# Kernel optimization log

Measured on AMD Instinct MI355X. Metric: run time of the kernel, lower is better.

The kernel has to match this reference:

```python
import jax, jax.numpy as jnp
import numpy as np

H, DH = 16, 64  # n_head, head_dim


def setup_inputs() -> dict:
    key = jax.random.key(0)
    ks = jax.random.split(key, 14)
    B, L, D = 2, 1024, 1024
    d = DH

    def lin_w(k, fan_in, shape):
        return jax.random.normal(k, shape, jnp.float32) / np.sqrt(fan_in)

    return {
        "x": jax.random.normal(ks[0], (B, L, D), jnp.float32),
        "Wq": lin_w(ks[1], D, (D, D)),
        "bq": jnp.zeros((D,), jnp.float32),
        "Wk1": lin_w(ks[2], D, (D, D)),
        "bk1": jnp.zeros((D,), jnp.float32),
        "Wk2": lin_w(ks[3], D, (D, D)),
        "bk2": jnp.zeros((D,), jnp.float32),
        "Wg": lin_w(ks[4], d, (d, 1)),
        "bg": jnp.zeros((1,), jnp.float32),
        "Ws": lin_w(ks[5], d, (d, 1)),
        "bs": jnp.zeros((1,), jnp.float32),
        "Wp": lin_w(ks[6], D, (D, D)),
        "bp": jnp.zeros((D,), jnp.float32),
    }


def reference(x, Wq, bq, Wk1, bk1, Wk2, bk2, Wg, bg, Ws, bs, Wp, bp):
    B, L, D = x.shape
    d = DH
    # AR (GLA) branch
    Q = (x @ Wq + bq).reshape(B, L, H, d)
    K = (x @ Wk1 + bk1).reshape(B, L, H, d)
    V = x.reshape(B, L, H, d)
    W = jnp.einsum('blhd,blhe->blhde', K, V)  # (B,L,H,d,d) outer products
    # stable cumprod of sigmoid gate via log-cumsum-exp trick
    G = jax.nn.sigmoid(x.reshape(B, L, H, d) @ Wg + bg)            # (B,L,H,1)
    log_cum = jnp.clip(jnp.cumsum(jnp.log(jnp.clip(G, 1e-6, None)), axis=1), -30.0, 30.0)
    Gc = (jnp.exp(log_cum) + 1e-6)[..., None]                       # (B,L,H,1,1)
    R = jax.nn.silu(K @ Ws + bs)[..., None]                         # (B,L,H,1,1) decay gate
    Wc = jnp.cumsum(W * R / Gc, axis=1) * Gc                        # weighted cumsum
    O1 = jnp.einsum('blhd,blhde->blhe', Q, Wc)                      # (B,L,H,d)
    # MA branch on one-step residuals
    E = V[:, 1:] - O1[:, :-1]                                       # (B,L-1,H,d)
    q2 = -jax.nn.leaky_relu(-Q[:, :-1] / np.sqrt(d), 0.02)          # ma_q_activation (scale head_dim)
    k2 = jax.nn.sigmoid((x[:, :-1] @ Wk2 + bk2) / np.sqrt(D) * 0.02)  # ma_k_activation (scale n_embd)
    k2 = k2.reshape(B, L - 1, H, d)
    W_ma = jnp.cumsum(jnp.einsum('blhd,blhe->blhde', k2, E), axis=1)
    O2 = jnp.einsum('blhd,blhde->blhe', q2, W_ma)
    O2 = jnp.concatenate([jnp.zeros_like(O2[:, :1]), O2], axis=1)   # shift: first MA output is 0
    O = (O1 + O2).reshape(B, L, D)
    return O @ Wp + bp
```

## Files before the change

### kernel.cpp

```cpp
#include <hip/hip_runtime.h>
#include <hip/hip_bf16.h>
#include <math.h>

#define B_  2
#define L_  1024
#define D_  1024
#define H_  16
#define DH_ 64
#define M_  (B_*L_)
#define CHUNK 64
#define NCH (L_/CHUNK)
#define PT 72
#define PS 76

#define KSCALE (0.02f/32.0f)

using bf16x8 = __attribute__((ext_vector_type(8))) short;
using f32x4  = __attribute__((ext_vector_type(4))) float;

__device__ __forceinline__ unsigned short bf16r(float f){
  union{float f; unsigned int u;} x; x.f = f;
  unsigned int r = x.u + 0x7FFF + ((x.u>>16)&1);
  return (unsigned short)(r>>16);
}
__device__ __forceinline__ float bf2f(unsigned short u){
  union{unsigned int u; float f;} x; x.u = ((unsigned int)u)<<16; return x.f;
}

__global__ __launch_bounds__(256) void convert_all(
  const float* __restrict__ X,
  const float* __restrict__ W0, const float* __restrict__ W1,
  const float* __restrict__ W2, const float* __restrict__ W3,
  unsigned short* __restrict__ Xbf,
  unsigned short* __restrict__ T0, unsigned short* __restrict__ T1,
  unsigned short* __restrict__ T2, unsigned short* __restrict__ T3)
{
  int z = blockIdx.z;
  if (z == 4) {
    int row = blockIdx.x*64 + (threadIdx.x>>2);
    int col = blockIdx.y*64 + (threadIdx.x&3)*16;
    const float4* src = (const float4*)&X[(size_t)row*D_ + col];
    float4 a=src[0], b=src[1], c=src[2], d=src[3];
    unsigned short buf[16] = {
      bf16r(a.x),bf16r(a.y),bf16r(a.z),bf16r(a.w),
      bf16r(b.x),bf16r(b.y),bf16r(b.z),bf16r(b.w),
      bf16r(c.x),bf16r(c.y),bf16r(c.z),bf16r(c.w),
      bf16r(d.x),bf16r(d.y),bf16r(d.z),bf16r(d.w)};
    *(uint4*)&Xbf[(size_t)row*D_ + col]     = *(uint4*)&buf[0];
    *(uint4*)&Xbf[(size_t)row*D_ + col + 8] = *(uint4*)&buf[8];
    return;
  }
  if (blockIdx.x >= 16) return;
  const float* W = z==0?W0: z==1?W1: z==2?W2: W3;
  unsigned short* T = z==0?T0: z==1?T1: z==2?T2: T3;
  __shared__ float tile[64][65];
  int kBase = blockIdx.x*64, nBase = blockIdx.y*64;
  #pragma unroll
  for (int i=0;i<16;i++){
    int idx = threadIdx.x + i*256;
    int r = idx>>6, c = idx&63;
    tile[r][c] = W[(size_t)(kBase+r)*D_ + nBase+c];
  }
  __syncthreads();
  #pragma unroll
  for (int i=0;i<16;i++){
    int idx = threadIdx.x + i*256;
    int n = idx>>6, k = idx&63;
    T[(size_t)(nBase+n)*D_ + kBase+k] = bf16r(tile[k][n]);
  }
}

__global__ __launch_bounds__(256) void gemm3(
  const unsigned short* __restrict__ A,
  const unsigned short* __restrict__ T0, const unsigned short* __restrict__ T1,
  const unsigned short* __restrict__ T2,
  const float* __restrict__ b0, const float* __restrict__ b1, const float* __restrict__ b2,
  unsigned short* __restrict__ F0, unsigned short* __restrict__ F1,
  unsigned short* __restrict__ F2)
{
  int z = blockIdx.z;
  const unsigned short* Bt = z==0?T0: z==1?T1: T2;
  const float* bias = z==0?b0: z==1?b1: b2;
  unsigned short* F = z==0?F0: z==1?F1: F2;
  int epi = (z==2) ? 1 : 0;
  int rowBase = blockIdx.x*128, colBase = blockIdx.y*128;

  __shared__ __align__(16) unsigned short As[128*32];
  __shared__ __align__(16) unsigned short Bs[128*32];
  int tid = threadIdx.x, w = tid>>6, l = tid&63;
  int lr = l&15, g4 = l>>4;
  int wr = w>>1, wc = w&1;
  f32x4 acc[4][4];
  #pragma unroll
  for (int mi=0;mi<4;mi++)
    #pragma unroll
    for (int ni=0;ni<4;ni++)
      acc[mi][ni] = (f32x4){0.f,0.f,0.f,0.f};

  for (int k0 = 0; k0 < D_; k0 += 32) {
    #pragma unroll
    for (int i=0;i<2;i++){
      int Fi = (w*2+i)*64 + l;
      int r = Fi>>2, c16 = Fi&3;
      int sc = c16 ^ ((r>>1)&3);
      const unsigned short* ga = A  + (size_t)(rowBase+r)*D_ + k0 + sc*8;
      const unsigned short* gb = Bt + (size_t)(colBase+r)*D_ + k0 + sc*8;
      __builtin_amdgcn_global_load_lds(
        (const __attribute__((address_space(1))) void*)ga,
        (__attribute__((address_space(3))) void*)(As + (size_t)(w*2+i)*512), 16, 0, 0);
      __builtin_amdgcn_global_load_lds(
        (const __attribute__((address_space(1))) void*)gb,
        (__attribute__((address_space(3))) void*)(Bs + (size_t)(w*2+i)*512), 16, 0, 0);
    }
    __syncthreads();
    bf16x8 af[4], bfr[4];
    #pragma unroll
    for (int mi=0;mi<4;mi++){
      int row = wr*64 + mi*16 + lr;
      af[mi] = *(const bf16x8*)(As + row*32 + ((g4 ^ ((row>>1)&3))*8));
    }
    #pragma unroll
    for (int ni=0;ni<4;ni++){
      int n = wc*64 + ni*16 + lr;
      bfr[ni] = *(const bf16x8*)(Bs + n*32 + ((g4 ^ ((n>>1)&3))*8));
    }
    #pragma unroll
    for (int mi=0;mi<4;mi++)
      #pragma unroll
      for (int ni=0;ni<4;ni++)
        acc[mi][ni] = __builtin_amdgcn_mfma_f32_16x16x32_bf16(af[mi], bfr[ni], acc[mi][ni], 0,0,0);
    __syncthreads();
  }

  #pragma unroll
  for (int mi=0;mi<4;mi++){
    #pragma unroll
    for (int ni=0;ni<4;ni++){
      int col = colBase + wc*64 + ni*16 + lr;
      float bv = bias[col];
      #pragma unroll
      for (int r=0;r<4;r++){
        int row = rowBase + wr*64 + mi*16 + g4*4 + r;
        float v = acc[mi][ni][r] + bv;
        if (epi) v = 1.f/(1.f + expf(-v*KSCALE));
        F[(size_t)row*D_ + col] = bf16r(v);
      }
    }
  }
}

__global__ __launch_bounds__(256) void gemm1(
  const unsigned short* __restrict__ A, const unsigned short* __restrict__ Bt,
  const float* __restrict__ bias, float* __restrict__ C)
{
  int rowBase = blockIdx.x*128, colBase = blockIdx.y*64;
  __shared__ __align__(16) unsigned short As[128*32];
  __shared__ __align__(16) unsigned short Bs[64*32];
  int tid = threadIdx.x, w = tid>>6, l = tid&63;
  int lr = l&15, g4 = l>>4;
  f32x4 acc[2][4];
  #pragma unroll
  for (int mi=0;mi<2;mi++)
    #pragma unroll
    for (int ni=0;ni<4;ni++)
      acc[mi][ni] = (f32x4){0.f,0.f,0.f,0.f};

  for (int k0 = 0; k0 < D_; k0 += 32) {
    #pragma unroll
    for (int i=0;i<2;i++){
      int F = (w*2+i)*64 + l;
      int r = F>>2, c16 = F&3;
      int sc = c16 ^ ((r>>1)&3);
      const unsigned short* g = A + (size_t)(rowBase+r)*D_ + k0 + sc*8;
      __builtin_amdgcn_global_load_lds(
        (const __attribute__((address_space(1))) void*)g,
        (__attribute__((address_space(3))) void*)(As + (size_t)(w*2+i)*512), 16, 0, 0);
    }
    {
      int F = w*64 + l;
      int r = F>>2, c16 = F&3;
      int sc = c16 ^ ((r>>1)&3);
      const unsigned short* g = Bt + (size_t)(colBase+r)*D_ + k0 + sc*8;
      __builtin_amdgcn_global_load_lds(
        (const __attribute__((address_space(1))) void*)g,
        (__attribute__((address_space(3))) void*)(Bs + (size_t)w*512), 16, 0, 0);
    }
    __syncthreads();
    bf16x8 af[2], bfr[4];
    #pragma unroll
    for (int mi=0;mi<2;mi++){
      int row = w*32 + mi*16 + lr;
      af[mi] = *(const bf16x8*)(As + row*32 + ((g4 ^ ((row>>1)&3))*8));
    }
    #pragma unroll
    for (int ni=0;ni<4;ni++){
      int n = ni*16 + lr;
      bfr[ni] = *(const bf16x8*)(Bs + n*32 + ((g4 ^ ((n>>1)&3))*8));
    }
    #pragma unroll
    for (int mi=0;mi<2;mi++)
      #pragma unroll
      for (int ni=0;ni<4;ni++)
        acc[mi][ni] = __builtin_amdgcn_mfma_f32_16x16x32_bf16(af[mi], bfr[ni], acc[mi][ni], 0,0,0);
    __syncthreads();
  }

  #pragma unroll
  for (int mi=0;mi<2;mi++){
    #pragma unroll
    for (int ni=0;ni<4;ni++){
      int col = colBase + ni*16 + lr;
      float bv = bias[col];
      #pragma unroll
      for (int r=0;r<4;r++){
        int row = rowBase + w*32 + mi*16 + g4*4 + r;
        C[(size_t)row*D_ + col] = acc[mi][ni][r] + bv;
      }
    }
  }
}

__global__ __launch_bounds__(256) void scalars_kernel(
  const float* __restrict__ X, const unsigned short* __restrict__ Kbf,
  const float* __restrict__ Wg, const float* __restrict__ bg,
  const float* __restrict__ Ws, const float* __restrict__ bs,
  float* __restrict__ GL, float* __restrict__ RR)
{
  int item = blockIdx.x * 4 + (threadIdx.x >> 6);
  int ln = threadIdx.x & 63;
  int row = item >> 4;
  int h = item & 15;
  float xv = X[(size_t)row*D_ + h*64 + ln];
  float kv = bf2f(Kbf[(size_t)row*D_ + h*64 + ln]);
  float gdot = xv * Wg[ln];
  float rdot = kv * Ws[ln];
  #pragma unroll
  for (int off = 32; off; off >>= 1) {
    gdot += __shfl_xor(gdot, off);
    rdot += __shfl_xor(rdot, off);
  }
  if (ln == 0) {
    float glogit = gdot + bg[0];
    float sg = 1.f/(1.f+expf(-glogit));
    sg = fmaxf(sg, 1e-6f);
    GL[item] = logf(sg);
    float rlogit = rdot + bs[0];
    RR[item] = rlogit / (1.f + expf(-rlogit));
  }
}

__global__ __launch_bounds__(256) void gl_scan(
  const float* __restrict__ GL, const float* __restrict__ RR,
  float* __restrict__ GC, float* __restrict__ CF)
{
  int bh = blockIdx.x * 4 + (threadIdx.x >> 6);
  int b = bh >> 4, h = bh & 15;
  int ln = threadIdx.x & 63;
  float carry = 0.f;
  for (int it = 0; it < 16; ++it) {
    int l = it*64 + ln;
    float x = GL[((size_t)(b*L_ + l))*H_ + h];
    #pragma unroll
    for (int off = 1; off < 64; off <<= 1) {
      float t = __shfl_up(x, off);
      if (ln >= off) x += t;
    }
    float tot = __shfl(x, 63);
    float cum = carry + x;
    carry += tot;
    float lc = fminf(fmaxf(cum, -30.f), 30.f);
    float gc = expf(lc) + 1e-6f;
    GC[(size_t)bh*L_ + l] = gc;
    CF[(size_t)bh*L_ + l] = RR[((size_t)(b*L_ + l))*H_ + h] / gc;
  }
}

__global__ __launch_bounds__(256) void ar_chunk_sum(
  const unsigned short* __restrict__ Kbf, const unsigned short* __restrict__ Xbf,
  const float* __restrict__ CF, float* __restrict__ CS)
{
  int bh = blockIdx.x, c = blockIdx.y;
  int b = bh >> 4, h = bh & 15;
  int row0 = b*L_ + c*CHUNK;
  __shared__ __align__(16) unsigned short kt_t[64*PT];
  __shared__ __align__(16) unsigned short cv_t[64*PT];
  __shared__ __align__(16) float uni[64*PS];
  __shared__ float cf_s[64];
  int tid = threadIdx.x;
  if (tid < 64) cf_s[tid] = CF[(size_t)bh*L_ + c*CHUNK + tid];
  __syncthreads();
  const unsigned short* kg = Kbf + (size_t)row0*D_ + h*64;
  const unsigned short* vg = Xbf + (size_t)row0*D_ + h*64;
  #pragma unroll
  for (int t=0;t<2;t++){
    int j = (tid>>3) + t*32;
    int d0 = (tid&7)*8;
    bf16x8 kv = *(const bf16x8*)&kg[(size_t)j*D_ + d0];
    bf16x8 vv = *(const bf16x8*)&vg[(size_t)j*D_ + d0];
    float cfj = cf_s[j];
    #pragma unroll
    for (int i=0;i<8;i++){
      kt_t[(d0+i)*PT + j] = (unsigned short)kv[i];
      cv_t[(d0+i)*PT + j] = bf16r(bf2f((unsigned short)vv[i]) * cfj);
    }
  }
  __syncthreads();
  int w = tid>>6, l = tid&63, lr = l&15, g4 = l>>4;
  f32x4 acc[4];
  #pragma unroll
  for (int ni=0;ni<4;ni++) acc[ni] = (f32x4){0.f,0.f,0.f,0.f};
  #pragma unroll
  for (int kk=0;kk<2;kk++){
    bf16x8 a = *(const bf16x8*)&cv_t[(w*16+lr)*PT + kk*32 + g4*8];
    #pragma unroll
    for (int ni=0;ni<4;ni++){
      bf16x8 bb = *(const bf16x8*)&kt_t[(ni*16+lr)*PT + kk*32 + g4*8];
      acc[ni] = __builtin_amdgcn_mfma_f32_16x16x32_bf16(a, bb, acc[ni], 0,0,0);
    }
  }
  #pragma unroll
  for (int ni=0;ni<4;ni++)
    #pragma unroll
    for (int r=0;r<4;r++)
      uni[(w*16+g4*4+r)*PS + ni*16+lr] = acc[ni][r];
  __syncthreads();
  float* out = CS + ((size_t)bh*NCH + c)*4096;
  #pragma unroll
  for (int t=0;t<4;t++){
    int idx = tid + t*256;
    int r = idx>>4, s = idx&15;
    *(float4*)&out[r*64 + s*4] = *(float4*)&uni[r*PS + s*4];
  }
}

__global__ __launch_bounds__(256) void ma_chunk_sum(
  const unsigned short* __restrict__ K2bf, const unsigned short* __restrict__ Xbf,
  const float* __restrict__ O1, float* __restrict__ CS)
{
  int bh = blockIdx.x, c = blockIdx.y;
  int b = bh >> 4, h = bh & 15;
  int row0 = b*L_ + c*CHUNK;
  __shared__ __align__(16) unsigned short kt_t[64*PT];
  __shared__ __align__(16) unsigned short et_t[64*PT];
  __shared__ __align__(16) float uni[64*PS];
  int tid = threadIdx.x;
  const unsigned short* kg = K2bf + (size_t)row0*D_ + h*64;
  #pragma unroll
  for (int t=0;t<2;t++){
    int j = (tid>>3) + t*32;
    int e0 = (tid&7)*8;
    bf16x8 kv = *(const bf16x8*)&kg[(size_t)j*D_ + e0];
    float ev[8] = {0.f,0.f,0.f,0.f,0.f,0.f,0.f,0.f};
    if (c*CHUNK + j < L_-1){
      bf16x8 xv = *(const bf16x8*)&Xbf[(size_t)(row0+j+1)*D_ + h*64 + e0];
      const float4* op = (const float4*)&O1[(size_t)(row0+j)*D_ + h*64 + e0];
      float4 o0 = op[0], o1v = op[1];
      ev[0]=bf2f((unsigned short)xv[0])-o0.x;  ev[1]=bf2f((unsigned short)xv[1])-o0.y;
      ev[2]=bf2f((unsigned short)xv[2])-o0.z;  ev[3]=bf2f((unsigned short)xv[3])-o0.w;
      ev[4]=bf2f((unsigned short)xv[4])-o1v.x; ev[5]=bf2f((unsigned short)xv[5])-o1v.y;
      ev[6]=bf2f((unsigned short)xv[6])-o1v.z; ev[7]=bf2f((unsigned short)xv[7])-o1v.w;
    }
    #pragma unroll
    for (int i=0;i<8;i++){
      kt_t[(e0+i)*PT + j] = (unsigned short)kv[i];
      et_t[(e0+i)*PT + j] = bf16r(ev[i]);
    }
  }
  __syncthreads();
  int w = tid>>6, l = tid&63, lr = l&15, g4 = l>>4;
  f32x4 acc[4];
  #pragma unroll
  for (int ni=0;ni<4;ni++) acc[ni] = (f32x4){0.f,0.f,0.f,0.f};
  #pragma unroll
  for (int kk=0;kk<2;kk++){
    bf16x8 a = *(const bf16x8*)&et_t[(w*16+lr)*PT + kk*32 + g4*8];
    #pragma unroll
    for (int ni=0;ni<4;ni++){
      bf16x8 bb = *(const bf16x8*)&kt_t[(ni*16+lr)*PT + kk*32 + g4*8];
      acc[ni] = __builtin_amdgcn_mfma_f32_16x16x32_bf16(a, bb, acc[ni], 0,0,0);
    }
  }
  #pragma unroll
  for (int ni=0;ni<4;ni++)
    #pragma unroll
    for (int r=0;r<4;r++)
      uni[(w*16+g4*4+r)*PS + ni*16+lr] = acc[ni][r];
  __syncthreads();
  float* out = CS + ((size_t)bh*NCH + c)*4096;
  #pragma unroll
  for (int t=0;t<4;t++){
    int idx = tid + t*256;
    int r = idx>>4, s = idx&15;
    *(float4*)&out[r*64 + s*4] = *(float4*)&uni[r*PS + s*4];
  }
}

__global__ __launch_bounds__(256) void ar_o1_mfma(
  const unsigned short* __restrict__ Qbf, const unsigned short* __restrict__ Kbf,
  const unsigned short* __restrict__ Xbf, const float* __restrict__ CF,
  const float* __restrict__ GC, const float* __restrict__ CS,
  float* __restrict__ O1)
{
  int bh = blockIdx.x, c = blockIdx.y;
  int b = bh >> 4, h = bh & 15;
  int row0 = b*L_ + c*CHUNK;
  __shared__ __align__(16) unsigned short q_t[64*PT];
  __shared__ __align__(16) unsigned short k_t[64*PT];
  __shared__ __align__(16) unsigned short vt_t[64*PT];
  __shared__ __align__(16) unsigned short st_t[64*PT];
  __shared__ __align__(16) float uni[64*PS];
  unsigned short* p_t = (unsigned short*)uni;
  __shared__ float cf_s[64], gc_s[64];
  int tid = threadIdx.x;
  if (tid < 64) {
    cf_s[tid] = CF[(size_t)bh*L_ + c*CHUNK + tid];
    gc_s[tid] = GC[(size_t)bh*L_ + c*CHUNK + tid];
  }
  const unsigned short* qg = Qbf + (size_t)row0*D_ + h*64;
  const unsigned short* kg = Kbf + (size_t)row0*D_ + h*64;
  const unsigned short* vg = Xbf + (size_t)row0*D_ + h*64;
  const float* csb = CS + (size_t)bh*NCH*4096;
  {
    float carry[16];
    #pragma unroll
    for (int i=0;i<16;i++) carry[i] = 0.f;
    const float* cb = csb + (size_t)tid*16;
    for (int c2=0;c2<c;c2++){
      const float4* p4 = (const float4*)(cb + (size_t)c2*4096);
      float4 a0=p4[0],a1=p4[1],a2=p4[2],a3=p4[3];
      carry[0]+=a0.x; carry[1]+=a0.y; carry[2]+=a0.z; carry[3]+=a0.w;
      carry[4]+=a1.x; carry[5]+=a1.y; carry[6]+=a1.z; carry[7]+=a1.w;
      carry[8]+=a2.x; carry[9]+=a2.y; carry[10]+=a2.z; carry[11]+=a2.w;
      carry[12]+=a3.x; carry[13]+=a3.y; carry[14]+=a3.z; carry[15]+=a3.w;
    }
    unsigned short buf[16];
    #pragma unroll
    for (int i=0;i<16;i++) buf[i] = bf16r(carry[i]);
    int row = tid>>2, col = (tid&3)*16;
    *(uint4*)&st_t[row*PT + col]     = *(uint4*)&buf[0];
    *(uint4*)&st_t[row*PT + col + 8] = *(uint4*)&buf[8];
  }
  #pragma unroll
  for (int t=0;t<2;t++){
    int idx = tid + t*256;
    int j = idx>>3, s = idx&7;
    *(uint4*)&q_t[j*PT + s*8] = *(const uint4*)&qg[(size_t)j*D_ + s*8];
    *(uint4*)&k_t[j*PT + s*8] = *(const uint4*)&kg[(size_t)j*D_ + s*8];
  }
  #pragma unroll
  for (int t=0;t<2;t++){
    int j = (tid>>3) + t*32;
    int e0 = (tid&7)*8;
    bf16x8 vv = *(const bf16x8*)&vg[(size_t)j*D_ + e0];
    #pragma unroll
    for (int i=0;i<8;i++) vt_t[(e0+i)*PT + j] = (unsigned short)vv[i];
  }
  __syncthreads();
  int w = tid>>6, l = tid&63, lr = l&15, g4 = l>>4;
  f32x4 acc[4];
  #pragma unroll
  for (int ni=0;ni<4;ni++) acc[ni] = (f32x4){0.f,0.f,0.f,0.f};
  #pragma unroll
  for (int kk=0;kk<2;kk++){
    bf16x8 a = *(const bf16x8*)&q_t[(w*16+lr)*PT + kk*32 + g4*8];
    #pragma unroll
    for (int ni=0;ni<4;ni++){
      bf16x8 bb = *(const bf16x8*)&k_t[(ni*16+lr)*PT + kk*32 + g4*8];
      acc[ni] = __builtin_amdgcn_mfma_f32_16x16x32_bf16(a, bb, acc[ni], 0,0,0);
    }
  }
  #pragma unroll
  for (int ni=0;ni<4;ni++){
    int j = ni*16 + lr;
    float cf = cf_s[j];
    #pragma unroll
    for (int r=0;r<4;r++){
      int row = w*16 + g4*4 + r;
      float v = (j <= row) ? acc[ni][r]*cf : 0.f;
      p_t[row*PT + j] = bf16r(v);
    }
  }
  __syncthreads();
  #pragma unroll
  for (int ni=0;ni<4;ni++) acc[ni] = (f32x4){0.f,0.f,0.f,0.f};
  #pragma unroll
  for (int kk=0;kk<2;kk++){
    bf16x8 ap = *(const bf16x8*)&p_t[(w*16+lr)*PT + kk*32 + g4*8];
    bf16x8 aq = *(const bf16x8*)&q_t[(w*16+lr)*PT + kk*32 + g4*8];
    #pragma unroll
    for (int ni=0;ni<4;ni++){
      bf16x8 bv = *(const bf16x8*)&vt_t[(ni*16+lr)*PT + kk*32 + g4*8];
      bf16x8 bs = *(const bf16x8*)&st_t[(ni*16+lr)*PT + kk*32 + g4*8];
      acc[ni] = __builtin_amdgcn_mfma_f32_16x16x32_bf16(ap, bv, acc[ni], 0,0,0);
      acc[ni] = __builtin_amdgcn_mfma_f32_16x16x32_bf16(aq, bs, acc[ni], 0,0,0);
    }
  }
  __syncthreads();
  #pragma unroll
  for (int ni=0;ni<4;ni++)
    #pragma unroll
    for (int r=0;r<4;r++){
      int row = w*16 + g4*4 + r;
      uni[row*PS + ni*16 + lr] = gc_s[row]*acc[ni][r];
    }
  __syncthreads();
  #pragma unroll
  for (int t=0;t<4;t++){
    int idx = tid + t*256;
    int r = idx>>4, s = idx&15;
    *(float4*)&O1[(size_t)(row0+r)*D_ + h*64 + s*4] = *(float4*)&uni[r*PS + s*4];
  }
}

__global__ __launch_bounds__(256) void ma_o2_mfma(
  const unsigned short* __restrict__ Qbf, const unsigned short* __restrict__ K2bf,
  const unsigned short* __restrict__ Xbf, const float* __restrict__ CS,
  const float* __restrict__ O1, unsigned short* __restrict__ Obf)
{
  int bh = blockIdx.x, c = blockIdx.y;
  int b = bh >> 4, h = bh & 15;
  int row0 = b*L_ + c*CHUNK;
  __shared__ __align__(16) unsigned short q_t[64*PT];
  __shared__ __align__(16) unsigned short k_t[64*PT];
  __shared__ __align__(16) unsigned short et_t[64*PT];
  __shared__ __align__(16) unsigned short tt_t[64*PT];
  __shared__ __align__(16) float uni[64*PS];
  unsigned short* p_t = (unsigned short*)uni;
  int tid = threadIdx.x;
  const unsigned short* qg = Qbf  + (size_t)row0*D_ + h*64;
  const unsigned short* kg = K2bf + (size_t)row0*D_ + h*64;
  const float* csb = CS + (size_t)bh*NCH*4096;
  {
    float carry[16];
    #pragma unroll
    for (int i=0;i<16;i++) carry[i] = 0.f;
    const float* cb = csb + (size_t)tid*16;
    for (int c2=0;c2<c;c2++){
      const float4* p4 = (const float4*)(cb + (size_t)c2*4096);
      float4 a0=p4[0],a1=p4[1],a2=p4[2],a3=p4[3];
      carry[0]+=a0.x; carry[1]+=a0.y; carry[2]+=a0.z; carry[3]+=a0.w;
      carry[4]+=a1.x; carry[5]+=a1.y; carry[6]+=a1.z; carry[7]+=a1.w;
      carry[8]+=a2.x; carry[9]+=a2.y; carry[10]+=a2.z; carry[11]+=a2.w;
      carry[12]+=a3.x; carry[13]+=a3.y; carry[14]+=a3.z; carry[15]+=a3.w;
    }
    unsigned short buf[16];
    #pragma unroll
    for (int i=0;i<16;i++) buf[i] = bf16r(carry[i]);
    int row = tid>>2, col = (tid&3)*16;
    *(uint4*)&tt_t[row*PT + col]     = *(uint4*)&buf[0];
    *(uint4*)&tt_t[row*PT + col + 8] = *(uint4*)&buf[8];
  }
  #pragma unroll
  for (int t=0;t<2;t++){
    int idx = tid + t*256;
    int j = idx>>3, s = idx&7;
    *(uint4*)&k_t[j*PT + s*8] = *(const uint4*)&kg[(size_t)j*D_ + s*8];
  }
  #pragma unroll
  for (int t=0;t<2;t++){
    int j = (tid>>3) + t*32;
    int d0 = (tid&7)*8;
    bf16x8 qv = *(const bf16x8*)&qg[(size_t)j*D_ + d0];
    unsigned short qb[8];
    #pragma unroll
    for (int i=0;i<8;i++){
      float q = bf2f((unsigned short)qv[i]);
      qb[i] = bf16r((q > 0.f ? 0.02f*q : q) * 0.125f);
    }
    *(uint4*)&q_t[j*PT + d0] = *(uint4*)&qb[0];
    float ev[8] = {0.f,0.f,0.f,0.f,0.f,0.f,0.f,0.f};
    if (c*CHUNK + j < L_-1){
      bf16x8 xv = *(const bf16x8*)&Xbf[(size_t)(row0+j+1)*D_ + h*64 + d0];
      const float4* op = (const float4*)&O1[(size_t)(row0+j)*D_ + h*64 + d0];
      float4 o0 = op[0], o1v = op[1];
      ev[0]=bf2f((unsigned short)xv[0])-o0.x;  ev[1]=bf2f((unsigned short)xv[1])-o0.y;
      ev[2]=bf2f((unsigned short)xv[2])-o0.z;  ev[3]=bf2f((unsigned short)xv[3])-o0.w;
      ev[4]=bf2f((unsigned short)xv[4])-o1v.x; ev[5]=bf2f((unsigned short)xv[5])-o1v.y;
      ev[6]=bf2f((unsigned short)xv[6])-o1v.z; ev[7]=bf2f((unsigned short)xv[7])-o1v.w;
    }
    #pragma unroll
    for (int i=0;i<8;i++) et_t[(d0+i)*PT + j] = bf16r(ev[i]);
  }
  __syncthreads();
  int w = tid>>6, l = tid&63, lr = l&15, g4 = l>>4;
  f32x4 acc[4];
  #pragma unroll
  for (int ni=0;ni<4;ni++) acc[ni] = (f32x4){0.f,0.f,0.f,0.f};
  #pragma unroll
  for (int kk=0;kk<2;kk++){
    bf16x8 a = *(const bf16x8*)&q_t[(w*16+lr)*PT + kk*32 + g4*8];
    #pragma unroll
    for (int ni=0;ni<4;ni++){
      bf16x8 bb = *(const bf16x8*)&k_t[(ni*16+lr)*PT + kk*32 + g4*8];
      acc[ni] = __builtin_amdgcn_mfma_f32_16x16x32_bf16(a, bb, acc[ni], 0,0,0);
    }
  }
  #pragma unroll
  for (int ni=0;ni<4;ni++){
    int j = ni*16 + lr;
    #pragma unroll
    for (int r=0;r<4;r++){
      int row = w*16 + g4*4 + r;
      float v = (j <= row) ? acc[ni][r] : 0.f;
      p_t[row*PT + j] = bf16r(v);
    }
  }
  __syncthreads();
  #pragma unroll
  for (int ni=0;ni<4;ni++) acc[ni] = (f32x4){0.f,0.f,0.f,0.f};
  #pragma unroll
  for (int kk=0;kk<2;kk++){
    bf16x8 ap = *(const bf16x8*)&p_t[(w*16+lr)*PT + kk*32 + g4*8];
    bf16x8 aq = *(const bf16x8*)&q_t[(w*16+lr)*PT + kk*32 + g4*8];
    #pragma unroll
    for (int ni=0;ni<4;ni++){
      bf16x8 be = *(const bf16x8*)&et_t[(ni*16+lr)*PT + kk*32 + g4*8];
      bf16x8 bt = *(const bf16x8*)&tt_t[(ni*16+lr)*PT + kk*32 + g4*8];
      acc[ni] = __builtin_amdgcn_mfma_f32_16x16x32_bf16(ap, be, acc[ni], 0,0,0);
      acc[ni] = __builtin_amdgcn_mfma_f32_16x16x32_bf16(aq, bt, acc[ni], 0,0,0);
    }
  }
  __syncthreads();
  #pragma unroll
  for (int ni=0;ni<4;ni++)
    #pragma unroll
    for (int r=0;r<4;r++){
      int row = w*16 + g4*4 + r;
      uni[row*PS + ni*16 + lr] = acc[ni][r];
    }
  __syncthreads();
  #pragma unroll
  for (int t=0;t<4;t++){
    int idx = tid + t*256;
    int r = idx>>4, s = idx&15;
    if (c*CHUNK + r < L_-1) {
      const float4 gv = *(const float4*)&O1[(size_t)(row0+r+1)*D_ + h*64 + s*4];
      float4 uv = *(float4*)&uni[r*PS + s*4];
      ushort4 o;
      o.x = bf16r(gv.x+uv.x); o.y = bf16r(gv.y+uv.y);
      o.z = bf16r(gv.z+uv.z); o.w = bf16r(gv.w+uv.w);
      *(ushort4*)&Obf[(size_t)(row0+r+1)*D_ + h*64 + s*4] = o;
    }
  }
  if (c == 0 && tid < 16) {
    const float4 gv = *(const float4*)&O1[(size_t)row0*D_ + h*64 + tid*4];
    ushort4 o;
    o.x = bf16r(gv.x); o.y = bf16r(gv.y); o.z = bf16r(gv.z); o.w = bf16r(gv.w);
    *(ushort4*)&Obf[(size_t)row0*D_ + h*64 + tid*4] = o;
  }
}

extern "C" void kernel_launch(void* const* d_in, const int* in_sizes, int n_in,
                              void* d_out, int out_size, void* d_ws, size_t ws_size,
                              hipStream_t stream) {
  const float* x  = (const float*)d_in[0];
  const float* Wq = (const float*)d_in[1];
  const float* bq = (const float*)d_in[2];
  const float* Wk1= (const float*)d_in[3];
  const float* bk1= (const float*)d_in[4];
  const float* Wk2= (const float*)d_in[5];
  const float* bk2= (const float*)d_in[6];
  const float* Wg = (const float*)d_in[7];
  const float* bg = (const float*)d_in[8];
  const float* Ws = (const float*)d_in[9];
  const float* bs = (const float*)d_in[10];
  const float* Wp = (const float*)d_in[11];
  const float* bp = (const float*)d_in[12];
  float* out = (float*)d_out;

  float* ws = (float*)d_ws;
  size_t MD = (size_t)M_*D_;
  float* O1b = ws;
  float* CSb = O1b + MD;
  float* GLb = CSb + (size_t)32*NCH*4096;
  float* RRb = GLb + (size_t)M_*H_;
  float* GCb = RRb + (size_t)M_*H_;
  float* CFb = GCb + (size_t)32*L_;
  unsigned short* Xbf   = (unsigned short*)(CFb + (size_t)32*L_);
  unsigned short* Qbfs  = Xbf  + MD;
  unsigned short* Kbfs  = Qbfs + MD;
  unsigned short* K2bfs = Kbfs + MD;
  unsigned short* Obf   = K2bfs+ MD;
  unsigned short* Wt0   = Obf + MD;
  unsigned short* Wt1   = Wt0 + (size_t)D_*D_;
  unsigned short* Wt2   = Wt1 + (size_t)D_*D_;
  unsigned short* Wt3   = Wt2 + (size_t)D_*D_;

  dim3 gcv(32, 16, 5);
  convert_all<<<gcv, 256, 0, stream>>>(x, Wq, Wk1, Wk2, Wp, Xbf, Wt0, Wt1, Wt2, Wt3);

  dim3 gg(M_/128, D_/128, 3);
  gemm3<<<gg, 256, 0, stream>>>(Xbf, Wt0, Wt1, Wt2, bq, bk1, bk2, Qbfs, Kbfs, K2bfs);

  scalars_kernel<<<(M_*H_)/4, 256, 0, stream>>>(x, Kbfs, Wg, bg, Ws, bs, GLb, RRb);
  gl_scan<<<8, 256, 0, stream>>>(GLb, RRb, GCb, CFb);

  dim3 gc(32, NCH);
  ar_chunk_sum<<<gc, 256, 0, stream>>>(Kbfs, Xbf, CFb, CSb);
  ar_o1_mfma<<<gc, 256, 0, stream>>>(Qbfs, Kbfs, Xbf, CFb, GCb, CSb, O1b);

  ma_chunk_sum<<<gc, 256, 0, stream>>>(K2bfs, Xbf, O1b, CSb);
  ma_o2_mfma<<<gc, 256, 0, stream>>>(Qbfs, K2bfs, Xbf, CSb, O1b, Obf);

  dim3 go(M_/128, D_/64);
  gemm1<<<go, 256, 0, stream>>>(Obf, Wt3, bp, out);
}
```

Measured before the change: 184.7 us.

## Fold gate scan into chunk kernels and fuse MA chunk sums into AR output

Removes the separate gate-scan kernel. Each chunk block now recomputes its own gate prefix, with one warp reducing the earlier chunks' log-gates, and GL/RR are stored head-major to make that read coalesced. The MA chunk-sum work moves into the AR output kernel, which builds the residual E from the O1 tile it already holds in shared memory instead of rereading O1 from global memory. This cuts two kernel launches and one global round trip of O1. In exchange, the prefix loop repeats work for later chunks and the fused kernel does more per block, with a longer serial tail.

```diff
diff --git a/kernel.cpp b/kernel.cpp
--- a/kernel.cpp
+++ b/kernel.cpp
@@ -25,6 +25,30 @@
 }
 __device__ __forceinline__ float bf2f(unsigned short u){
   union{unsigned int u; float f;} x; x.u = ((unsigned int)u)<<16; return x.f;
+}
+
+__device__ __forceinline__ void gate_prefix(
+  const float* __restrict__ GL, const float* __restrict__ RR,
+  int bh, int c, int l, float* cf_s, float* gc_s)
+{
+  float carry = 0.f;
+  for (int it = 0; it < c; ++it){
+    float g = GL[(size_t)bh*L_ + it*64 + l];
+    #pragma unroll
+    for (int off = 32; off; off >>= 1) g += __shfl_xor(g, off);
+    carry += g;
+  }
+  float x = GL[(size_t)bh*L_ + c*64 + l];
+  #pragma unroll
+  for (int off = 1; off < 64; off <<= 1){
+    float t = __shfl_up(x, off);
+    if (l >= off) x += t;
+  }
+  float cum = carry + x;
+  float lc = fminf(fmaxf(cum, -30.f), 30.f);
+  float gc = expf(lc) + 1e-6f;
+  cf_s[l] = RR[(size_t)bh*L_ + c*64 + l] / gc;
+  if (gc_s) gc_s[l] = gc;
 }
 
 __global__ __launch_bounds__(256) void convert_all(
@@ -240,44 +264,21 @@
     rdot += __shfl_xor(rdot, off);
   }
   if (ln == 0) {
+    int b = row >> 10, l = row & 1023;
+    size_t o = (size_t)(b*16 + h)*L_ + l;
     float glogit = gdot + bg[0];
     float sg = 1.f/(1.f+expf(-glogit));
     sg = fmaxf(sg, 1e-6f);
-    GL[item] = logf(sg);
+    GL[o] = logf(sg);
     float rlogit = rdot + bs[0];
-    RR[item] = rlogit / (1.f + expf(-rlogit));
-  }
-}
-
-__global__ __launch_bounds__(256) void gl_scan(
-  const float* __restrict__ GL, const float* __restrict__ RR,
-  float* __restrict__ GC, float* __restrict__ CF)
-{
-  int bh = blockIdx.x * 4 + (threadIdx.x >> 6);
-  int b = bh >> 4, h = bh & 15;
-  int ln = threadIdx.x & 63;
-  float carry = 0.f;
-  for (int it = 0; it < 16; ++it) {
-    int l = it*64 + ln;
-    float x = GL[((size_t)(b*L_ + l))*H_ + h];
-    #pragma unroll
-    for (int off = 1; off < 64; off <<= 1) {
-      float t = __shfl_up(x, off);
-      if (ln >= off) x += t;
-    }
-    float tot = __shfl(x, 63);
-    float cum = carry + x;
-    carry += tot;
-    float lc = fminf(fmaxf(cum, -30.f), 30.f);
-    float gc = expf(lc) + 1e-6f;
-    GC[(size_t)bh*L_ + l] = gc;
-    CF[(size_t)bh*L_ + l] = RR[((size_t)(b*L_ + l))*H_ + h] / gc;
+    RR[o] = rlogit / (1.f + expf(-rlogit));
   }
 }
 
 __global__ __launch_bounds__(256) void ar_chunk_sum(
   const unsigned short* __restrict__ Kbf, const unsigned short* __restrict__ Xbf,
-  const float* __restrict__ CF, float* __restrict__ CS)
+  const float* __restrict__ GL, const float* __restrict__ RR,
+  float* __restrict__ CS)
 {
   int bh = blockIdx.x, c = blockIdx.y;
   int b = bh >> 4, h = bh & 15;
@@ -287,7 +288,7 @@
   __shared__ __align__(16) float uni[64*PS];
   __shared__ float cf_s[64];
   int tid = threadIdx.x;
-  if (tid < 64) cf_s[tid] = CF[(size_t)bh*L_ + c*CHUNK + tid];
+  if (tid < 64) gate_prefix(GL, RR, bh, c, tid, cf_s, nullptr);
   __syncthreads();
   const unsigned short* kg = Kbf + (size_t)row0*D_ + h*64;
   const unsigned short* vg = Xbf + (size_t)row0*D_ + h*64;
@@ -333,72 +334,11 @@
   }
 }
 
-__global__ __launch_bounds__(256) void ma_chunk_sum(
-  const unsigned short* __restrict__ K2bf, const unsigned short* __restrict__ Xbf,
-  const float* __restrict__ O1, float* __restrict__ CS)
-{
-  int bh = blockIdx.x, c = blockIdx.y;
-  int b = bh >> 4, h = bh & 15;
-  int row0 = b*L_ + c*CHUNK;
-  __shared__ __align__(16) unsigned short kt_t[64*PT];
-  __shared__ __align__(16) unsigned short et_t[64*PT];
-  __shared__ __align__(16) float uni[64*PS];
-  int tid = threadIdx.x;
-  const unsigned short* kg = K2bf + (size_t)row0*D_ + h*64;
-  #pragma unroll
-  for (int t=0;t<2;t++){
-    int j = (tid>>3) + t*32;
-    int e0 = (tid&7)*8;
-    bf16x8 kv = *(const bf16x8*)&kg[(size_t)j*D_ + e0];
-    float ev[8] = {0.f,0.f,0.f,0.f,0.f,0.f,0.f,0.f};
-    if (c*CHUNK + j < L_-1){
-      bf16x8 xv = *(const bf16x8*)&Xbf[(size_t)(row0+j+1)*D_ + h*64 + e0];
-      const float4* op = (const float4*)&O1[(size_t)(row0+j)*D_ + h*64 + e0];
-      float4 o0 = op[0], o1v = op[1];
-      ev[0]=bf2f((unsigned short)xv[0])-o0.x;  ev[1]=bf2f((unsigned short)xv[1])-o0.y;
-      ev[2]=bf2f((unsigned short)xv[2])-o0.z;  ev[3]=bf2f((unsigned short)xv[3])-o0.w;
-      ev[4]=bf2f((unsigned short)xv[4])-o1v.x; ev[5]=bf2f((unsigned short)xv[5])-o1v.y;
-      ev[6]=bf2f((unsigned short)xv[6])-o1v.z; ev[7]=bf2f((unsigned short)xv[7])-o1v.w;
-    }
-    #pragma unroll
-    for (int i=0;i<8;i++){
-      kt_t[(e0+i)*PT + j] = (unsigned short)kv[i];
-      et_t[(e0+i)*PT + j] = bf16r(ev[i]);
-    }
-  }
-  __syncthreads();
-  int w = tid>>6, l = tid&63, lr = l&15, g4 = l>>4;
-  f32x4 acc[4];
-  #pragma unroll
-  for (int ni=0;ni<4;ni++) acc[ni] = (f32x4){0.f,0.f,0.f,0.f};
-  #pragma unroll
-  for (int kk=0;kk<2;kk++){
-    bf16x8 a = *(const bf16x8*)&et_t[(w*16+lr)*PT + kk*32 + g4*8];
-    #pragma unroll
-    for (int ni=0;ni<4;ni++){
-      bf16x8 bb = *(const bf16x8*)&kt_t[(ni*16+lr)*PT + kk*32 + g4*8];
-      acc[ni] = __builtin_amdgcn_mfma_f32_16x16x32_bf16(a, bb, acc[ni], 0,0,0);
-    }
-  }
-  #pragma unroll
-  for (int ni=0;ni<4;ni++)
-    #pragma unroll
-    for (int r=0;r<4;r++)
-      uni[(w*16+g4*4+r)*PS + ni*16+lr] = acc[ni][r];
-  __syncthreads();
-  float* out = CS + ((size_t)bh*NCH + c)*4096;
-  #pragma unroll
-  for (int t=0;t<4;t++){
-    int idx = tid + t*256;
-    int r = idx>>4, s = idx&15;
-    *(float4*)&out[r*64 + s*4] = *(float4*)&uni[r*PS + s*4];
-  }
-}
-
-__global__ __launch_bounds__(256) void ar_o1_mfma(
+__global__ __launch_bounds__(256) void ar_o1_fused(
   const unsigned short* __restrict__ Qbf, const unsigned short* __restrict__ Kbf,
-  const unsigned short* __restrict__ Xbf, const float* __restrict__ CF,
-  const float* __restrict__ GC, const float* __restrict__ CS,
+  const unsigned short* __restrict__ Xbf, const unsigned short* __restrict__ K2bf,
+  const float* __restrict__ GL, const float* __restrict__ RR,
+  const float* __restrict__ CSA, float* __restrict__ CSM,
   float* __restrict__ O1)
 {
   int bh = blockIdx.x, c = blockIdx.y;
@@ -412,14 +352,11 @@
   unsigned short* p_t = (unsigned short*)uni;
   __shared__ float cf_s[64], gc_s[64];
   int tid = threadIdx.x;
-  if (tid < 64) {
-    cf_s[tid] = CF[(size_t)bh*L_ + c*CHUNK + tid];
-    gc_s[tid] = GC[(size_t)bh*L_ + c*CHUNK + tid];
-  }
+  if (tid < 64) gate_prefix(GL, RR, bh, c, tid, cf_s, gc_s);
   const unsigned short* qg = Qbf + (size_t)row0*D_ + h*64;
   const unsigned short* kg = Kbf + (size_t)row0*D_ + h*64;
   const unsigned short* vg = Xbf + (size_t)row0*D_ + h*64;
-  const float* csb = CS + (size_t)bh*NCH*4096;
+  const float* csb = CSA + (size_t)bh*NCH*4096;
   {
     float carry[16];
     #pragma unroll
@@ -509,6 +446,49 @@
     int idx = tid + t*256;
     int r = idx>>4, s = idx&15;
     *(float4*)&O1[(size_t)(row0+r)*D_ + h*64 + s*4] = *(float4*)&uni[r*PS + s*4];
+  }
+  #pragma unroll
+  for (int t=0;t<2;t++){
+    int j = (tid>>3) + t*32;
+    int d0 = (tid&7)*8;
+    bf16x8 kv = *(const bf16x8*)&K2bf[(size_t)(row0+j)*D_ + h*64 + d0];
+    float ev[8] = {0.f,0.f,0.f,0.f,0.f,0.f,0.f,0.f};
+    if (c*CHUNK + j < L_-1){
+      bf16x8 xv = *(const bf16x8*)&Xbf[(size_t)(row0+j+1)*D_ + h*64 + d0];
+      #pragma unroll
+      for (int i=0;i<8;i++) ev[i] = bf2f((unsigned short)xv[i]) - uni[j*PS + d0 + i];
+    }
+    #pragma unroll
+    for (int i=0;i<8;i++){
+      vt_t[(d0+i)*PT + j] = (unsigned short)kv[i];
+      k_t [(d0+i)*PT + j] = bf16r(ev[i]);
+    }
+  }
+  __syncthreads();
+  f32x4 acc2[4];
+  #pragma unroll
+  for (int ni=0;ni<4;ni++) acc2[ni] = (f32x4){0.f,0.f,0.f,0.f};
+  #pragma unroll
+  for (int kk=0;kk<2;kk++){
+    bf16x8 a = *(const bf16x8*)&k_t[(w*16+lr)*PT + kk*32 + g4*8];
+    #pragma unroll
+    for (int ni=0;ni<4;ni++){
+      bf16x8 bb = *(const bf16x8*)&vt_t[(ni*16+lr)*PT + kk*32 + g4*8];
+      acc2[ni] = __builtin_amdgcn_mfma_f32_16x16x32_bf16(a, bb, acc2[ni], 0,0,0);
+    }
+  }
+  #pragma unroll
+  for (int ni=0;ni<4;ni++)
+    #pragma unroll
+    for (int r=0;r<4;r++)
+      uni[(w*16+g4*4+r)*PS + ni*16+lr] = acc2[ni][r];
+  __syncthreads();
+  float* outm = CSM + ((size_t)bh*NCH + c)*4096;
+  #pragma unroll
+  for (int t=0;t<4;t++){
+    int idx = tid + t*256;
+    int r = idx>>4, s = idx&15;
+    *(float4*)&outm[r*64 + s*4] = *(float4*)&uni[r*PS + s*4];
   }
 }
 
@@ -671,12 +651,11 @@
   float* ws = (float*)d_ws;
   size_t MD = (size_t)M_*D_;
   float* O1b = ws;
-  float* CSb = O1b + MD;
-  float* GLb = CSb + (size_t)32*NCH*4096;
-  float* RRb = GLb + (size_t)M_*H_;
-  float* GCb = RRb + (size_t)M_*H_;
-  float* CFb = GCb + (size_t)32*L_;
-  unsigned short* Xbf   = (unsigned short*)(CFb + (size_t)32*L_);
+  float* CSA = O1b + MD;
+  float* CSM = CSA + (size_t)32*NCH*4096;
+  float* GLb = CSM + (size_t)32*NCH*4096;
+  float* RRb = GLb + (size_t)32*L_;
+  unsigned short* Xbf   = (unsigned short*)(RRb + (size_t)32*L_);
   unsigned short* Qbfs  = Xbf  + MD;
   unsigned short* Kbfs  = Qbfs + MD;
   unsigned short* K2bfs = Kbfs + MD;
@@ -693,14 +672,11 @@
   gemm3<<<gg, 256, 0, stream>>>(Xbf, Wt0, Wt1, Wt2, bq, bk1, bk2, Qbfs, Kbfs, K2bfs);
 
   scalars_kernel<<<(M_*H_)/4, 256, 0, stream>>>(x, Kbfs, Wg, bg, Ws, bs, GLb, RRb);
-  gl_scan<<<8, 256, 0, stream>>>(GLb, RRb, GCb, CFb);
 
   dim3 gc(32, NCH);
-  ar_chunk_sum<<<gc, 256, 0, stream>>>(Kbfs, Xbf, CFb, CSb);
-  ar_o1_mfma<<<gc, 256, 0, stream>>>(Qbfs, Kbfs, Xbf, CFb, GCb, CSb, O1b);
-
-  ma_chunk_sum<<<gc, 256, 0, stream>>>(K2bfs, Xbf, O1b, CSb);
-  ma_o2_mfma<<<gc, 256, 0, stream>>>(Qbfs, K2bfs, Xbf, CSb, O1b, Obf);
+  ar_chunk_sum<<<gc, 256, 0, stream>>>(Kbfs, Xbf, GLb, RRb, CSA);
+  ar_o1_fused<<<gc, 256, 0, stream>>>(Qbfs, Kbfs, Xbf, K2bfs, GLb, RRb, CSA, CSM, O1b);
+  ma_o2_mfma<<<gc, 256, 0, stream>>>(Qbfs, K2bfs, Xbf, CSM, O1b, Obf);
 
   dim3 go(M_/128, D_/64);
   gemm1<<<go, 256, 0, stream>>>(Obf, Wt3, bp, out);
```

After: 185.2 us. Within noise of the previous version (+0.3%).
